# Kernel optimization log

Hardware: AMD Instinct MI355X
Metric: run time of the kernel (lower is better)

Reference implementation:

```python
import jax, jax.numpy as jnp
from jax import lax
import numpy as np

EPS = 1e-8


def _pdist(a):
    # torch.cdist(a, a, p=2): pairwise Euclidean distances [B, B]
    sq = jnp.sum(a * a, axis=1)
    d2 = sq[:, None] + sq[None, :] - 2.0 * (a @ a.T)
    d2 = jnp.maximum(d2, 0.0)
    # safe sqrt: zero distance -> 0 with zero (not NaN) gradient
    pos = d2 > 0
    return jnp.where(pos, jnp.sqrt(jnp.where(pos, d2, 1.0)), 0.0)


def _local_curvature(x, k):
    # PCA-residual curvature per sample: 1 - S0 / sum(S) over k-NN neighborhood
    dists = _pdist(x)                          # [B, B]
    _, knn_idx = lax.top_k(-dists, k + 1)      # smallest k+1 distances
    knn_idx = knn_idx[:, 1:]                   # drop self -> [B, k]
    nbrs = x[knn_idx]                          # [B, k, D] gather
    centered = nbrs - jnp.mean(nbrs, axis=1, keepdims=True)
    S = jnp.linalg.svd(centered, compute_uv=False)  # batched singular values [B, k]
    linearity = S[:, 0] / (jnp.sum(S, axis=1) + EPS)
    return 1.0 - linearity                     # [B]


def reference(z, ref_emb, x_original, k):
    B = z.shape[0]
    curv = _local_curvature(x_original, k)     # [B]
    z_dist = _pdist(z)
    ref_dist = _pdist(ref_emb)
    # weights = clamp(1 - max(curv_i, curv_j), min=0.1)
    weights = jnp.maximum(1.0 - jnp.maximum(curv[:, None], curv[None, :]), 0.1)
    z_norm = z_dist / (jnp.max(z_dist) + EPS)
    ref_norm = ref_dist / (jnp.max(ref_dist) + EPS)
    errors = (z_norm - ref_norm) ** 2 * weights
    mask = jnp.triu(jnp.ones((B, B), dtype=bool), k=1)
    n_pairs = B * (B - 1) / 2.0
    return jnp.sum(jnp.where(mask, errors, 0.0)) / n_pairs


def setup_inputs() -> dict:
    key = jax.random.key(0)
    k1, k2, k3 = jax.random.split(key, 3)
    B, D, DZ, DR = 4096, 1024, 128, 128
    return {
        "z": jax.random.normal(k1, (B, DZ), dtype=jnp.float32),
        "ref_emb": jax.random.normal(k2, (B, DR), dtype=jnp.float32),
        "x_original": jax.random.normal(k3, (B, D), dtype=jnp.float32),
        "k": 10,
    }
```

## Files before the change

### kernel.cpp

```cpp
#include <hip/hip_runtime.h>
#include <math.h>

#define NB 4096
#define DX 1024
#define DZ 128
#define KNN 10
#define STR 32
#define NLIST 32
#define BKK 64
#define NSTEP (DX / BKK)

typedef short short8v __attribute__((ext_vector_type(8)));
typedef float f32x4 __attribute__((ext_vector_type(4)));

#define MFMA16(a, b, c) __builtin_amdgcn_mfma_f32_16x16x32_bf16((a), (b), (c), 0, 0, 0)

__device__ __forceinline__ ushort f2bf(float f) {
  unsigned u = __float_as_uint(f);
  u += 0x7FFFu + ((u >> 16) & 1u);
  return (ushort)(u >> 16);
}
__device__ __forceinline__ float bf2f(ushort h) {
  return __uint_as_float(((unsigned)h) << 16);
}

__device__ __forceinline__ void gload16(const ushort* g, ushort* l) {
  __builtin_amdgcn_global_load_lds(
      (const __attribute__((address_space(1))) void*)g,
      (__attribute__((address_space(3))) void*)l, 16, 0, 0);
}

__device__ __forceinline__ short8v frag_ld(const ushort* base, int row, int fg) {
  int off = (row << 6) + (fg << 4);
  off ^= (row & 7) << 4;
  return *(const short8v*)((const char*)base + off);
}

__device__ __forceinline__ int swz64(int row, int c8) {
  return (row << 7) + ((c8 ^ (row & 7)) << 4);
}
__device__ __forceinline__ short8v frag_ld64(const ushort* base, int row, int kk, int fg) {
  return *(const short8v*)((const char*)base + swz64(row, kk * 4 + fg));
}

#define INSERT10(td, ti, v, idx)                         \
  do {                                                   \
    if ((v) < td[KNN - 1]) {                             \
      _Pragma("unroll")                                  \
      for (int k_ = KNN - 1; k_ >= 1; --k_) {            \
        bool bk = (v) < td[k_];                          \
        bool bk1 = (v) < td[k_ - 1];                     \
        td[k_] = bk ? (bk1 ? td[k_ - 1] : (v)) : td[k_]; \
        ti[k_] = bk ? (bk1 ? ti[k_ - 1] : (idx)) : ti[k_]; \
      }                                                  \
      bool b0 = (v) < td[0];                             \
      ti[0] = b0 ? (idx) : ti[0];                        \
      td[0] = b0 ? (v) : td[0];                          \
    }                                                    \
  } while (0)

__global__ __launch_bounds__(256) void k_rowsq(const float* __restrict__ a,
                                               float* __restrict__ out, int D) {
  int row = blockIdx.x;
  const float4* p = (const float4*)(a + (size_t)row * D);
  float s = 0.f;
  for (int d = threadIdx.x; d < (D >> 2); d += 256) {
    float4 v = p[d];
    s = fmaf(v.x, v.x, s); s = fmaf(v.y, v.y, s);
    s = fmaf(v.z, v.z, s); s = fmaf(v.w, v.w, s);
  }
#pragma unroll
  for (int m = 32; m; m >>= 1) s += __shfl_xor(s, m);
  __shared__ float red[4];
  int w = threadIdx.x >> 6;
  if ((threadIdx.x & 63) == 0) red[w] = s;
  __syncthreads();
  if (threadIdx.x == 0) out[row] = red[0] + red[1] + red[2] + red[3];
}

__global__ __launch_bounds__(256) void k_prep_x(const float* __restrict__ x,
                                                ushort* __restrict__ xh,
                                                float* __restrict__ sqx) {
  const int row = blockIdx.x, t = threadIdx.x;
  float4 v = ((const float4*)(x + (size_t)row * DX))[t];
  ushort4 hv;
  hv.x = f2bf(v.x); hv.y = f2bf(v.y); hv.z = f2bf(v.z); hv.w = f2bf(v.w);
  ((ushort4*)(xh + (size_t)row * DX))[t] = hv;
  float s = fmaf(v.x, v.x, fmaf(v.y, v.y, fmaf(v.z, v.z, v.w * v.w)));
#pragma unroll
  for (int m = 32; m; m >>= 1) s += __shfl_xor(s, m);
  __shared__ float red[4];
  int w = t >> 6;
  if ((t & 63) == 0) red[w] = s;
  __syncthreads();
  if (t == 0) sqx[row] = red[0] + red[1] + red[2] + red[3];
}

__global__ __launch_bounds__(256) void k_prep_zr(const float* __restrict__ z,
                                                 const float* __restrict__ rfm,
                                                 ushort* __restrict__ zh, ushort* __restrict__ zl,
                                                 ushort* __restrict__ rh, ushort* __restrict__ rl,
                                                 float* __restrict__ sqz, float* __restrict__ sqr) {
  const float* src = blockIdx.y ? rfm : z;
  ushort* ph = blockIdx.y ? rh : zh;
  ushort* pl = blockIdx.y ? rl : zl;
  float* sq = blockIdx.y ? sqr : sqz;
  const int t = threadIdx.x;
  const size_t base = (size_t)blockIdx.x * 1024;
  float4 v = ((const float4*)(src + base))[t];
  float vv[4] = {v.x, v.y, v.z, v.w};
  ushort h[4], l[4];
#pragma unroll
  for (int e = 0; e < 4; ++e) {
    h[e] = f2bf(vv[e]);
    l[e] = f2bf(vv[e] - bf2f(h[e]));
  }
  ushort4 hv; hv.x = h[0]; hv.y = h[1]; hv.z = h[2]; hv.w = h[3];
  ushort4 lv; lv.x = l[0]; lv.y = l[1]; lv.z = l[2]; lv.w = l[3];
  ((ushort4*)(ph + base))[t] = hv;
  ((ushort4*)(pl + base))[t] = lv;
  float s = fmaf(v.x, v.x, fmaf(v.y, v.y, fmaf(v.z, v.z, v.w * v.w)));
#pragma unroll
  for (int m = 16; m; m >>= 1) s += __shfl_xor(s, m);
  if ((t & 31) == 0) sq[blockIdx.x * 8 + (t >> 5)] = s;
}

struct SmemKNN {
  union {
    struct { ushort A[2][8192]; ushort B[2][8192]; } s;
    float D[64 * 129];
  } u;
};

template<int PRE>
__global__ __launch_bounds__(256, 2) void k_knn(const float* __restrict__ x,
                                                const ushort* __restrict__ xh,
                                                const float* __restrict__ sqx,
                                                float* __restrict__ cand_d,
                                                int* __restrict__ cand_i) {
  __shared__ SmemKNN sm;
  const int bid = blockIdx.y * STR + blockIdx.x;
  const int xcd = bid & 7, rr = bid >> 3;
  const int strip = (xcd & 3) * 8 + (rr & 7);
  const int itile = (xcd >> 2) * 16 + (rr >> 3);
  const int i0 = itile * 128;
  const int j0 = strip * 128;

  const int tid = threadIdx.x;
  const int lane = tid & 63, wv = tid >> 6;
  const int wr = wv >> 1, wc = wv & 1;
  const int fr = lane & 15, fg = lane >> 4;

  float td[KNN];
  int ti[KNN];
#pragma unroll
  for (int k = 0; k < KNN; ++k) { td[k] = 3.0e38f; ti[k] = 0; }
  const int my_chunk = tid >> 7;
  const int t2 = tid & 127;
  const int srow = t2 >> 1;
  const int cbase = (tid & 1) * 64;

  f32x4 acc[4][4];
  const f32x4 zv4 = {0.f, 0.f, 0.f, 0.f};
#pragma unroll
  for (int m = 0; m < 4; ++m)
#pragma unroll
    for (int n = 0; n < 4; ++n) acc[m][n] = zv4;

  if (PRE) {
    const int lr = lane >> 3;
    const int lc8 = (lane & 7) ^ lr;
#define ISSUE_TILE(kc, buf)                                                  \
  _Pragma("unroll")                                                          \
  for (int c_ = 0; c_ < 4; ++c_) {                                          \
    int ch_ = wv * 4 + c_;                                                   \
    int row_ = ch_ * 8 + lr;                                                 \
    gload16(xh + (size_t)(i0 + row_) * DX + (kc) + lc8 * 8,                  \
            &sm.u.s.A[buf][ch_ * 512]);                                      \
    gload16(xh + (size_t)(j0 + row_) * DX + (kc) + lc8 * 8,                  \
            &sm.u.s.B[buf][ch_ * 512]);                                      \
  }
    ISSUE_TILE(0, 0);
    int buf = 0;
    for (int step = 0; step < NSTEP; ++step) {
      asm volatile("s_waitcnt vmcnt(0)" ::: "memory");
      __syncthreads();
      if (step + 1 < NSTEP) ISSUE_TILE((step + 1) * BKK, buf ^ 1);
      const ushort* Ab = sm.u.s.A[buf];
      const ushort* Bb = sm.u.s.B[buf];
#pragma unroll
      for (int kk = 0; kk < 2; ++kk) {
        short8v fa[4];
#pragma unroll
        for (int m = 0; m < 4; ++m)
          fa[m] = frag_ld64(Ab, wr * 64 + m * 16 + fr, kk, fg);
#pragma unroll
        for (int n = 0; n < 4; ++n) {
          short8v fb = frag_ld64(Bb, wc * 64 + n * 16 + fr, kk, fg);
#pragma unroll
          for (int m = 0; m < 4; ++m)
            acc[m][n] = MFMA16(fa[m], fb, acc[m][n]);
        }
      }
      buf ^= 1;
    }
#undef ISSUE_TILE
  } else {
    for (int kc = 0; kc < DX; kc += BKK) {
      __syncthreads();
#pragma unroll
      for (int l = 0; l < 4; ++l) {
        int idx = tid + l * 256;
        int row = idx >> 3, c8 = idx & 7;
        int off = swz64(row, c8);
        const float* pa = &x[(size_t)(i0 + row) * DX + kc + c8 * 8];
        const float* pb = &x[(size_t)(j0 + row) * DX + kc + c8 * 8];
        float4 a1 = *(const float4*)pa, a2 = *(const float4*)(pa + 4);
        float4 b1 = *(const float4*)pb, b2 = *(const float4*)(pb + 4);
        uint4 pva, pvb;
        pva.x = (unsigned)f2bf(a1.x) | ((unsigned)f2bf(a1.y) << 16);
        pva.y = (unsigned)f2bf(a1.z) | ((unsigned)f2bf(a1.w) << 16);
        pva.z = (unsigned)f2bf(a2.x) | ((unsigned)f2bf(a2.y) << 16);
        pva.w = (unsigned)f2bf(a2.z) | ((unsigned)f2bf(a2.w) << 16);
        pvb.x = (unsigned)f2bf(b1.x) | ((unsigned)f2bf(b1.y) << 16);
        pvb.y = (unsigned)f2bf(b1.z) | ((unsigned)f2bf(b1.w) << 16);
        pvb.z = (unsigned)f2bf(b2.x) | ((unsigned)f2bf(b2.y) << 16);
        pvb.w = (unsigned)f2bf(b2.z) | ((unsigned)f2bf(b2.w) << 16);
        *(uint4*)((char*)sm.u.s.A[0] + off) = pva;
        *(uint4*)((char*)sm.u.s.B[0] + off) = pvb;
      }
      __syncthreads();
#pragma unroll
      for (int kk = 0; kk < 2; ++kk) {
        short8v fa[4];
#pragma unroll
        for (int m = 0; m < 4; ++m)
          fa[m] = frag_ld64(sm.u.s.A[0], wr * 64 + m * 16 + fr, kk, fg);
#pragma unroll
        for (int n = 0; n < 4; ++n) {
          short8v fb = frag_ld64(sm.u.s.B[0], wc * 64 + n * 16 + fr, kk, fg);
#pragma unroll
          for (int m = 0; m < 4; ++m)
            acc[m][n] = MFMA16(fa[m], fb, acc[m][n]);
        }
      }
    }
  }
  __syncthreads();
#pragma unroll
  for (int chunk = 0; chunk < 2; ++chunk) {
    if (wr == chunk) {
#pragma unroll
      for (int m = 0; m < 4; ++m)
#pragma unroll
        for (int n = 0; n < 4; ++n)
#pragma unroll
          for (int r = 0; r < 4; ++r) {
            int rl = m * 16 + fg * 4 + r;
            int cl = wc * 64 + n * 16 + fr;
            int gi = i0 + chunk * 64 + rl, gj = j0 + cl;
            float v = sqx[gi] + sqx[gj] - 2.f * acc[m][n][r];
            sm.u.D[rl * 129 + cl] = (gi == gj) ? 3.0e38f : v;
          }
    }
    __syncthreads();
    if (my_chunk == chunk) {
#pragma unroll 4
      for (int c = 0; c < 64; ++c) {
        float v = sm.u.D[srow * 129 + cbase + c];
        int idx = j0 + cbase + c;
        INSERT10(td, ti, v, idx);
      }
    }
    __syncthreads();
  }
  {
    float pd[KNN]; int pi[KNN];
#pragma unroll
    for (int l = 0; l < KNN; ++l) {
      pd[l] = __shfl_xor(td[l], 1);
      pi[l] = __shfl_xor(ti[l], 1);
    }
#pragma unroll
    for (int l = 0; l < KNN; ++l) INSERT10(td, ti, pd[l], pi[l]);
    if ((tid & 1) == 0) {
      int row = i0 + my_chunk * 64 + srow;
#pragma unroll
      for (int l = 0; l < KNN; ++l) {
        cand_d[((size_t)row * NLIST + strip) * KNN + l] = td[l];
        cand_i[((size_t)row * NLIST + strip) * KNN + l] = ti[l];
      }
    }
  }
}

template<int PRE>
__global__ __launch_bounds__(64) void k_mergegram(const float* __restrict__ cand_d,
                                                  const int* __restrict__ cand_i,
                                                  const float* __restrict__ x,
                                                  const ushort* __restrict__ xh,
                                                  float* __restrict__ G) {
  const int pt = blockIdx.x;
  const int lane = threadIdx.x;
  float v[KNN]; int jx[KNN];
  const float* cd = cand_d + ((size_t)pt * NLIST + lane) * KNN;
  const int* ci = cand_i + ((size_t)pt * NLIST + lane) * KNN;
  const bool act = lane < NLIST;
#pragma unroll
  for (int l = 0; l < KNN; ++l) {
    v[l] = act ? cd[l] : 3.0e38f;
    jx[l] = act ? ci[l] : 0;
  }
  int nbi[KNN];
#pragma unroll
  for (int k = 0; k < KNN; ++k) {
    float bv = v[0]; int bj = jx[0]; int bl = lane;
#pragma unroll
    for (int m = 1; m < 64; m <<= 1) {
      float ov = __shfl_xor(bv, m);
      int oj = __shfl_xor(bj, m);
      int ol = __shfl_xor(bl, m);
      bool take = ov < bv;
      bv = take ? ov : bv; bj = take ? oj : bj; bl = take ? ol : bl;
    }
    nbi[k] = bj;
    if (lane == bl) {
#pragma unroll
      for (int l = 0; l < KNN - 1; ++l) { v[l] = v[l + 1]; jx[l] = jx[l + 1]; }
      v[KNN - 1] = 3.0e38f;
    }
  }
  float P[55];
  float U[KNN];
  float q = 0.f;
#pragma unroll
  for (int c = 0; c < 55; ++c) P[c] = 0.f;
#pragma unroll
  for (int a = 0; a < KNN; ++a) U[a] = 0.f;
  if (PRE) {
    const short8v* nb[KNN];
#pragma unroll
    for (int a = 0; a < KNN; ++a)
      nb[a] = (const short8v*)(xh + (size_t)nbi[a] * DX);
    for (int d8 = lane; d8 < DX / 8; d8 += 64) {
      short8v n8[KNN];
#pragma unroll
      for (int a = 0; a < KNN; ++a) n8[a] = nb[a][d8];
#pragma unroll
      for (int e = 0; e < 8; ++e) {
        float n[KNN];
#pragma unroll
        for (int a = 0; a < KNN; ++a) n[a] = bf2f((ushort)n8[a][e]);
        float m = 0.f;
#pragma unroll
        for (int a = 0; a < KNN; ++a) m += n[a];
        m *= 0.1f;
        q = fmaf(m, m, q);
#pragma unroll
        for (int a = 0; a < KNN; ++a) U[a] = fmaf(n[a], m, U[a]);
        int c = 0;
#pragma unroll
        for (int a = 0; a < KNN; ++a)
#pragma unroll
          for (int b = a; b < KNN; ++b) { P[c] = fmaf(n[a], n[b], P[c]); ++c; }
      }
    }
  } else {
    const float4* nb[KNN];
#pragma unroll
    for (int a = 0; a < KNN; ++a)
      nb[a] = (const float4*)(x + (size_t)nbi[a] * DX);
    for (int d4 = lane; d4 < DX / 4; d4 += 64) {
      float4 n4[KNN];
#pragma unroll
      for (int a = 0; a < KNN; ++a) n4[a] = nb[a][d4];
#pragma unroll
      for (int e = 0; e < 4; ++e) {
        float n[KNN];
#pragma unroll
        for (int a = 0; a < KNN; ++a) n[a] = ((const float*)&n4[a])[e];
        float m = 0.f;
#pragma unroll
        for (int a = 0; a < KNN; ++a) m += n[a];
        m *= 0.1f;
        q = fmaf(m, m, q);
#pragma unroll
        for (int a = 0; a < KNN; ++a) U[a] = fmaf(n[a], m, U[a]);
        int c = 0;
#pragma unroll
        for (int a = 0; a < KNN; ++a)
#pragma unroll
          for (int b = a; b < KNN; ++b) { P[c] = fmaf(n[a], n[b], P[c]); ++c; }
      }
    }
  }
#pragma unroll
  for (int c = 0; c < 55; ++c)
#pragma unroll
    for (int m2 = 32; m2; m2 >>= 1) P[c] += __shfl_xor(P[c], m2);
#pragma unroll
  for (int a = 0; a < KNN; ++a)
#pragma unroll
    for (int m2 = 32; m2; m2 >>= 1) U[a] += __shfl_xor(U[a], m2);
#pragma unroll
  for (int m2 = 32; m2; m2 >>= 1) q += __shfl_xor(q, m2);
  if (lane == 0) {
    int c = 0;
    for (int a = 0; a < KNN; ++a)
      for (int b = a; b < KNN; ++b) { G[(size_t)pt * 55 + c] = P[c] - U[a] - U[b] + q; ++c; }
  }
}

__device__ __forceinline__ constexpr int IJ(int a, int b) {
  return (a <= b) ? (10 * a - (a * (a - 1)) / 2 + (b - a))
                  : (10 * b - (b * (b - 1)) / 2 + (a - b));
}

#define NSWEEP 6
__global__ __launch_bounds__(64) void k_jacobi(const float* __restrict__ G,
                                               float* __restrict__ curv) {
  const int pt = blockIdx.x * 64 + threadIdx.x;
  float M[55];
#pragma unroll
  for (int c = 0; c < 55; ++c) M[c] = G[(size_t)pt * 55 + c];

#pragma unroll
  for (int sweep = 0; sweep < NSWEEP; ++sweep) {
#pragma unroll
    for (int p = 0; p < KNN - 1; ++p) {
#pragma unroll
      for (int q = p + 1; q < KNN; ++q) {
        float apq = M[IJ(p, q)];
        float app = M[IJ(p, p)], aqq = M[IJ(q, q)];
        float theta = (aqq - app) / (2.f * apq);
        float t = 1.f / (fabsf(theta) + sqrtf(fmaf(theta, theta, 1.f)));
        t = (theta < 0.f) ? -t : t;
        t = (apq == 0.f) ? 0.f : t;
        float cc = 1.f / sqrtf(fmaf(t, t, 1.f));
        float ss = t * cc;
#pragma unroll
        for (int r = 0; r < KNN; ++r) {
          if (r == p || r == q) continue;
          float vrp = M[IJ(r, p)];
          float vrq = M[IJ(r, q)];
          M[IJ(r, p)] = cc * vrp - ss * vrq;
          M[IJ(r, q)] = ss * vrp + cc * vrq;
        }
        M[IJ(p, p)] = app - t * apq;
        M[IJ(q, q)] = aqq + t * apq;
        M[IJ(p, q)] = 0.f;
      }
    }
  }

  float lmax = 0.f, ssum = 0.f;
#pragma unroll
  for (int a = 0; a < KNN; ++a) {
    float l = fmaxf(M[IJ(a, a)], 0.f);
    lmax = fmaxf(lmax, l);
    ssum += sqrtf(l);
  }
  curv[pt] = 1.f - sqrtf(lmax) / (ssum + 1e-8f);
}

template<int PRE>
__global__ __launch_bounds__(256, 2) void k_zr(const float* __restrict__ z,
                                               const float* __restrict__ rfm,
                                               const ushort* __restrict__ zh,
                                               const ushort* __restrict__ zl,
                                               const ushort* __restrict__ rh,
                                               const ushort* __restrict__ rl,
                                               const float* __restrict__ sqz,
                                               const float* __restrict__ sqr,
                                               const float* __restrict__ curv,
                                               double* __restrict__ pS,
                                               float* __restrict__ pM) {
  __shared__ struct { ushort Ah[4096], Al[4096], Bh[4096], Bl[4096]; } s;
  const int t = blockIdx.x;
  int ib = 0, base = 0;
  while (base + (32 - ib) <= t) { base += 32 - ib; ++ib; }
  const int jb = ib + (t - base);
  const int i0 = ib * 128, j0 = jb * 128;
  const int tid = threadIdx.x;
  const int lane = tid & 63, wv = tid >> 6;
  const int wr = wv >> 1, wc = wv & 1;
  const int fr = lane & 15, fg = lane >> 4;

  f32x4 zacc[4][4], racc[4][4];
  const f32x4 zv = {0.f, 0.f, 0.f, 0.f};
#pragma unroll
  for (int m = 0; m < 4; ++m)
#pragma unroll
    for (int n = 0; n < 4; ++n) { zacc[m][n] = zv; racc[m][n] = zv; }

#pragma unroll
  for (int mat = 0; mat < 2; ++mat) {
    const float* P = mat ? rfm : z;
    const ushort* Ph = mat ? rh : zh;
    const ushort* Pl = mat ? rl : zl;
    for (int kc = 0; kc < DZ; kc += 32) {
      __syncthreads();
      if (PRE) {
#pragma unroll
        for (int l = 0; l < 2; ++l) {
          int idx = tid + l * 256;
          int row = idx >> 2, c8 = idx & 3;
          int off = (row << 6) + (c8 << 4);
          off ^= (row & 7) << 4;
          size_t ga = (size_t)(i0 + row) * DZ + kc + c8 * 8;
          size_t gb = (size_t)(j0 + row) * DZ + kc + c8 * 8;
          *(uint4*)((char*)s.Ah + off) = *(const uint4*)(Ph + ga);
          *(uint4*)((char*)s.Al + off) = *(const uint4*)(Pl + ga);
          *(uint4*)((char*)s.Bh + off) = *(const uint4*)(Ph + gb);
          *(uint4*)((char*)s.Bl + off) = *(const uint4*)(Pl + gb);
        }
      } else {
#pragma unroll
        for (int l = 0; l < 4; ++l) {
          int idx = tid + l * 256;
          int row = idx >> 3, c4 = idx & 7;
          int off = (row << 6) + (c4 << 3);
          off ^= (row & 7) << 4;
          float4 va = *(const float4*)&P[(size_t)(i0 + row) * DZ + kc + c4 * 4];
          float4 vb = *(const float4*)&P[(size_t)(j0 + row) * DZ + kc + c4 * 4];
          float av[4] = {va.x, va.y, va.z, va.w};
          float bv[4] = {vb.x, vb.y, vb.z, vb.w};
          ushort ah4[4], al4[4], bh4[4], bl4[4];
#pragma unroll
          for (int e = 0; e < 4; ++e) {
            ah4[e] = f2bf(av[e]); al4[e] = f2bf(av[e] - bf2f(ah4[e]));
            bh4[e] = f2bf(bv[e]); bl4[e] = f2bf(bv[e] - bf2f(bh4[e]));
          }
          uint2 p;
          p.x = (unsigned)ah4[0] | ((unsigned)ah4[1] << 16);
          p.y = (unsigned)ah4[2] | ((unsigned)ah4[3] << 16);
          *(uint2*)((char*)s.Ah + off) = p;
          p.x = (unsigned)al4[0] | ((unsigned)al4[1] << 16);
          p.y = (unsigned)al4[2] | ((unsigned)al4[3] << 16);
          *(uint2*)((char*)s.Al + off) = p;
          p.x = (unsigned)bh4[0] | ((unsigned)bh4[1] << 16);
          p.y = (unsigned)bh4[2] | ((unsigned)bh4[3] << 16);
          *(uint2*)((char*)s.Bh + off) = p;
          p.x = (unsigned)bl4[0] | ((unsigned)bl4[1] << 16);
          p.y = (unsigned)bl4[2] | ((unsigned)bl4[3] << 16);
          *(uint2*)((char*)s.Bl + off) = p;
        }
      }
      __syncthreads();
      short8v fah[4], fal[4];
#pragma unroll
      for (int m = 0; m < 4; ++m) {
        int r = wr * 64 + m * 16 + fr;
        fah[m] = frag_ld(s.Ah, r, fg);
        fal[m] = frag_ld(s.Al, r, fg);
      }
#pragma unroll
      for (int n = 0; n < 4; ++n) {
        int r = wc * 64 + n * 16 + fr;
        short8v fbh = frag_ld(s.Bh, r, fg);
        short8v fbl = frag_ld(s.Bl, r, fg);
#pragma unroll
        for (int m = 0; m < 4; ++m) {
          if (mat == 0) {
            zacc[m][n] = MFMA16(fah[m], fbh, zacc[m][n]);
            zacc[m][n] = MFMA16(fah[m], fbl, zacc[m][n]);
            zacc[m][n] = MFMA16(fal[m], fbh, zacc[m][n]);
          } else {
            racc[m][n] = MFMA16(fah[m], fbh, racc[m][n]);
            racc[m][n] = MFMA16(fah[m], fbl, racc[m][n]);
            racc[m][n] = MFMA16(fal[m], fbh, racc[m][n]);
          }
        }
      }
    }
  }

  double s1 = 0, s2 = 0, s3 = 0;
  float mz = 0.f, mr = 0.f;
#pragma unroll
  for (int m = 0; m < 4; ++m)
#pragma unroll
    for (int n = 0; n < 4; ++n)
#pragma unroll
      for (int r = 0; r < 4; ++r) {
        int gi = i0 + wr * 64 + m * 16 + fg * 4 + r;
        int gj = j0 + wc * 64 + n * 16 + fr;
        if (gj > gi) {
          float z2 = fmaxf(sqz[gi] + sqz[gj] - 2.f * zacc[m][n][r], 0.f);
          float r2 = fmaxf(sqr[gi] + sqr[gj] - 2.f * racc[m][n][r], 0.f);
          float w = fmaxf(1.f - fmaxf(curv[gi], curv[gj]), 0.1f);
          s1 += (double)(w * z2);
          s3 += (double)(w * r2);
          s2 += (double)(w * sqrtf(z2 * r2));
          mz = fmaxf(mz, z2);
          mr = fmaxf(mr, r2);
        }
      }
#pragma unroll
  for (int m = 32; m; m >>= 1) {
    s1 += __shfl_xor(s1, m);
    s2 += __shfl_xor(s2, m);
    s3 += __shfl_xor(s3, m);
    mz = fmaxf(mz, __shfl_xor(mz, m));
    mr = fmaxf(mr, __shfl_xor(mr, m));
  }
  __shared__ double rd[4][3];
  __shared__ float rf2[4][2];
  int w = tid >> 6;
  if ((tid & 63) == 0) { rd[w][0] = s1; rd[w][1] = s2; rd[w][2] = s3; rf2[w][0] = mz; rf2[w][1] = mr; }
  __syncthreads();
  if (tid == 0) {
    double a = 0, b = 0, c = 0; float d = 0.f, e = 0.f;
    for (int i = 0; i < 4; ++i) {
      a += rd[i][0]; b += rd[i][1]; c += rd[i][2];
      d = fmaxf(d, rf2[i][0]); e = fmaxf(e, rf2[i][1]);
    }
    pS[(size_t)t * 3 + 0] = a; pS[(size_t)t * 3 + 1] = b; pS[(size_t)t * 3 + 2] = c;
    pM[(size_t)t * 2 + 0] = d; pM[(size_t)t * 2 + 1] = e;
  }
}

__global__ __launch_bounds__(256) void k_final(const double* __restrict__ pS,
                                               const float* __restrict__ pM,
                                               int nb, float* __restrict__ out) {
  int tid = threadIdx.x;
  double s1 = 0, s2 = 0, s3 = 0; float mz = 0.f, mr = 0.f;
  for (int i = tid; i < nb; i += 256) {
    s1 += pS[(size_t)i * 3 + 0]; s2 += pS[(size_t)i * 3 + 1]; s3 += pS[(size_t)i * 3 + 2];
    mz = fmaxf(mz, pM[(size_t)i * 2 + 0]); mr = fmaxf(mr, pM[(size_t)i * 2 + 1]);
  }
#pragma unroll
  for (int m = 32; m; m >>= 1) {
    s1 += __shfl_xor(s1, m); s2 += __shfl_xor(s2, m); s3 += __shfl_xor(s3, m);
    mz = fmaxf(mz, __shfl_xor(mz, m)); mr = fmaxf(mr, __shfl_xor(mr, m));
  }
  __shared__ double rd[4][3];
  __shared__ float rf2[4][2];
  int w = tid >> 6;
  if ((tid & 63) == 0) { rd[w][0] = s1; rd[w][1] = s2; rd[w][2] = s3; rf2[w][0] = mz; rf2[w][1] = mr; }
  __syncthreads();
  if (tid == 0) {
    double a = 0, b = 0, c = 0; float d = 0.f, e = 0.f;
    for (int i = 0; i < 4; ++i) {
      a += rd[i][0]; b += rd[i][1]; c += rd[i][2];
      d = fmaxf(d, rf2[i][0]); e = fmaxf(e, rf2[i][1]);
    }
    double zm = sqrt((double)d) + 1e-8;
    double rm = sqrt((double)e) + 1e-8;
    double total = a / (zm * zm) - 2.0 * b / (zm * rm) + c / (rm * rm);
    double npairs = (double)NB * (double)(NB - 1) / 2.0;
    out[0] = (float)(total / npairs);
  }
}

extern "C" void kernel_launch(void* const* d_in, const int* in_sizes, int n_in,
                              void* d_out, int out_size, void* d_ws, size_t ws_size,
                              hipStream_t stream) {
  const float* z = (const float*)d_in[0];
  const float* rfm = (const float*)d_in[1];
  const float* x = (const float*)d_in[2];
  float* out = (float*)d_out;
  char* w = (char*)d_ws;

  float*  sqx    = (float*)(w + 0);
  float*  sqz    = (float*)(w + 16384);
  float*  sqr    = (float*)(w + 32768);
  float*  curv   = (float*)(w + 49152);
  float*  cand_d = (float*)(w + 229376);
  int*    cand_i = (int*)(w + 5472256);
  float*  G      = (float*)(w + 10715136);
  double* pS     = (double*)(w + 11616256);
  float*  pM     = (float*)(w + 11628928);

  ushort* xh = (ushort*)(w + (size_t)12 * 1024 * 1024);
  ushort* zh = (ushort*)(w + (size_t)20 * 1024 * 1024);
  ushort* zl = (ushort*)(w + (size_t)21 * 1024 * 1024);
  ushort* rh = (ushort*)(w + (size_t)22 * 1024 * 1024);
  ushort* rl = (ushort*)(w + (size_t)23 * 1024 * 1024);
  const bool pre = ws_size >= (size_t)24 * 1024 * 1024;

  if (pre) {
    k_prep_x<<<NB, 256, 0, stream>>>(x, xh, sqx);
    k_prep_zr<<<dim3(NB * DZ / 1024, 2), 256, 0, stream>>>(z, rfm, zh, zl, rh, rl, sqz, sqr);
    k_knn<1><<<dim3(STR, NB / 128), 256, 0, stream>>>(x, xh, sqx, cand_d, cand_i);
    k_mergegram<1><<<NB, 64, 0, stream>>>(cand_d, cand_i, x, xh, G);
  } else {
    k_rowsq<<<NB, 256, 0, stream>>>(x, sqx, DX);
    k_rowsq<<<NB, 256, 0, stream>>>(z, sqz, DZ);
    k_rowsq<<<NB, 256, 0, stream>>>(rfm, sqr, DZ);
    k_knn<0><<<dim3(STR, NB / 128), 256, 0, stream>>>(x, xh, sqx, cand_d, cand_i);
    k_mergegram<0><<<NB, 64, 0, stream>>>(cand_d, cand_i, x, xh, G);
  }
  k_jacobi<<<NB / 64, 64, 0, stream>>>(G, curv);
  if (pre) {
    k_zr<1><<<528, 256, 0, stream>>>(z, rfm, zh, zl, rh, rl, sqz, sqr, curv, pS, pM);
  } else {
    k_zr<0><<<528, 256, 0, stream>>>(z, rfm, zh, zl, rh, rl, sqz, sqr, curv, pS, pM);
  }
  k_final<<<1, 256, 0, stream>>>(pS, pM, 528, out);
}
```

Measured before the change: 263.0 us.

## Enlarge kNN GEMM tile to 256x128 with 512 threads, drop async LDS double buffering

The kNN distance GEMM block tile grows from 128x128 to 256x128, using 8 waves per block and half as many blocks, so each B strip loaded into shared memory is reused across more rows. The precomputed-bf16 path loses its global_load_lds double-buffered pipeline and now uses plain synchronous vector loads into a single buffer, sharing one loop with the fp32 path. This cuts redundant B traffic but exposes load latency with no overlap. The epilogue now runs 4 row chunks through the 64x129 staging buffer.

After: 267.6 us. No clear change (+1.8%).

```diff
diff --git a/kernel.cpp b/kernel.cpp
--- a/kernel.cpp
+++ b/kernel.cpp
@@ -8,7 +8,6 @@
 #define STR 32
 #define NLIST 32
 #define BKK 64
-#define NSTEP (DX / BKK)
 
 typedef short short8v __attribute__((ext_vector_type(8)));
 typedef float f32x4 __attribute__((ext_vector_type(4)));
@@ -22,12 +21,6 @@
 }
 __device__ __forceinline__ float bf2f(ushort h) {
   return __uint_as_float(((unsigned)h) << 16);
-}
-
-__device__ __forceinline__ void gload16(const ushort* g, ushort* l) {
-  __builtin_amdgcn_global_load_lds(
-      (const __attribute__((address_space(1))) void*)g,
-      (__attribute__((address_space(3))) void*)l, 16, 0, 0);
 }
 
 __device__ __forceinline__ short8v frag_ld(const ushort* base, int row, int fg) {
@@ -127,13 +120,13 @@
 
 struct SmemKNN {
   union {
-    struct { ushort A[2][8192]; ushort B[2][8192]; } s;
+    struct { ushort A[256 * BKK], B[128 * BKK]; } s;
     float D[64 * 129];
   } u;
 };
 
 template<int PRE>
-__global__ __launch_bounds__(256, 2) void k_knn(const float* __restrict__ x,
+__global__ __launch_bounds__(512, 4) void k_knn(const float* __restrict__ x,
                                                 const ushort* __restrict__ xh,
                                                 const float* __restrict__ sqx,
                                                 float* __restrict__ cand_d,
@@ -142,8 +135,8 @@
   const int bid = blockIdx.y * STR + blockIdx.x;
   const int xcd = bid & 7, rr = bid >> 3;
   const int strip = (xcd & 3) * 8 + (rr & 7);
-  const int itile = (xcd >> 2) * 16 + (rr >> 3);
-  const int i0 = itile * 128;
+  const int itile = (xcd >> 2) * 8 + (rr >> 3);
+  const int i0 = itile * 256;
   const int j0 = strip * 128;
 
   const int tid = threadIdx.x;
@@ -167,88 +160,70 @@
 #pragma unroll
     for (int n = 0; n < 4; ++n) acc[m][n] = zv4;
 
-  if (PRE) {
-    const int lr = lane >> 3;
-    const int lc8 = (lane & 7) ^ lr;
-#define ISSUE_TILE(kc, buf)                                                  \
-  _Pragma("unroll")                                                          \
-  for (int c_ = 0; c_ < 4; ++c_) {                                          \
-    int ch_ = wv * 4 + c_;                                                   \
-    int row_ = ch_ * 8 + lr;                                                 \
-    gload16(xh + (size_t)(i0 + row_) * DX + (kc) + lc8 * 8,                  \
-            &sm.u.s.A[buf][ch_ * 512]);                                      \
-    gload16(xh + (size_t)(j0 + row_) * DX + (kc) + lc8 * 8,                  \
-            &sm.u.s.B[buf][ch_ * 512]);                                      \
-  }
-    ISSUE_TILE(0, 0);
-    int buf = 0;
-    for (int step = 0; step < NSTEP; ++step) {
-      asm volatile("s_waitcnt vmcnt(0)" ::: "memory");
-      __syncthreads();
-      if (step + 1 < NSTEP) ISSUE_TILE((step + 1) * BKK, buf ^ 1);
-      const ushort* Ab = sm.u.s.A[buf];
-      const ushort* Bb = sm.u.s.B[buf];
-#pragma unroll
-      for (int kk = 0; kk < 2; ++kk) {
-        short8v fa[4];
-#pragma unroll
-        for (int m = 0; m < 4; ++m)
-          fa[m] = frag_ld64(Ab, wr * 64 + m * 16 + fr, kk, fg);
-#pragma unroll
-        for (int n = 0; n < 4; ++n) {
-          short8v fb = frag_ld64(Bb, wc * 64 + n * 16 + fr, kk, fg);
-#pragma unroll
-          for (int m = 0; m < 4; ++m)
-            acc[m][n] = MFMA16(fa[m], fb, acc[m][n]);
-        }
-      }
-      buf ^= 1;
-    }
-#undef ISSUE_TILE
-  } else {
-    for (int kc = 0; kc < DX; kc += BKK) {
-      __syncthreads();
+  for (int kc = 0; kc < DX; kc += BKK) {
+    __syncthreads();
+    if (PRE) {
 #pragma unroll
       for (int l = 0; l < 4; ++l) {
-        int idx = tid + l * 256;
+        int idx = tid + l * 512;
         int row = idx >> 3, c8 = idx & 7;
-        int off = swz64(row, c8);
+        *(uint4*)((char*)sm.u.s.A + swz64(row, c8)) =
+            *(const uint4*)(xh + (size_t)(i0 + row) * DX + kc + c8 * 8);
+      }
+#pragma unroll
+      for (int l = 0; l < 2; ++l) {
+        int idx = tid + l * 512;
+        int row = idx >> 3, c8 = idx & 7;
+        *(uint4*)((char*)sm.u.s.B + swz64(row, c8)) =
+            *(const uint4*)(xh + (size_t)(j0 + row) * DX + kc + c8 * 8);
+      }
+    } else {
+#pragma unroll
+      for (int l = 0; l < 4; ++l) {
+        int idx = tid + l * 512;
+        int row = idx >> 3, c8 = idx & 7;
         const float* pa = &x[(size_t)(i0 + row) * DX + kc + c8 * 8];
-        const float* pb = &x[(size_t)(j0 + row) * DX + kc + c8 * 8];
         float4 a1 = *(const float4*)pa, a2 = *(const float4*)(pa + 4);
-        float4 b1 = *(const float4*)pb, b2 = *(const float4*)(pb + 4);
-        uint4 pva, pvb;
+        uint4 pva;
         pva.x = (unsigned)f2bf(a1.x) | ((unsigned)f2bf(a1.y) << 16);
         pva.y = (unsigned)f2bf(a1.z) | ((unsigned)f2bf(a1.w) << 16);
         pva.z = (unsigned)f2bf(a2.x) | ((unsigned)f2bf(a2.y) << 16);
         pva.w = (unsigned)f2bf(a2.z) | ((unsigned)f2bf(a2.w) << 16);
+        *(uint4*)((char*)sm.u.s.A + swz64(row, c8)) = pva;
+      }
+#pragma unroll
+      for (int l = 0; l < 2; ++l) {
+        int idx = tid + l * 512;
+        int row = idx >> 3, c8 = idx & 7;
+        const float* pb = &x[(size_t)(j0 + row) * DX + kc + c8 * 8];
+        float4 b1 = *(const float4*)pb, b2 = *(const float4*)(pb + 4);
+        uint4 pvb;
         pvb.x = (unsigned)f2bf(b1.x) | ((unsigned)f2bf(b1.y) << 16);
         pvb.y = (unsigned)f2bf(b1.z) | ((unsigned)f2bf(b1.w) << 16);
         pvb.z = (unsigned)f2bf(b2.x) | ((unsigned)f2bf(b2.y) << 16);
         pvb.w = (unsigned)f2bf(b2.z) | ((unsigned)f2bf(b2.w) << 16);
-        *(uint4*)((char*)sm.u.s.A[0] + off) = pva;
-        *(uint4*)((char*)sm.u.s.B[0] + off) = pvb;
-      }
-      __syncthreads();
-#pragma unroll
-      for (int kk = 0; kk < 2; ++kk) {
-        short8v fa[4];
+        *(uint4*)((char*)sm.u.s.B + swz64(row, c8)) = pvb;
+      }
+    }
+    __syncthreads();
+#pragma unroll
+    for (int kk = 0; kk < 2; ++kk) {
+      short8v fa[4];
+#pragma unroll
+      for (int m = 0; m < 4; ++m)
+        fa[m] = frag_ld64(sm.u.s.A, wr * 64 + m * 16 + fr, kk, fg);
+#pragma unroll
+      for (int n = 0; n < 4; ++n) {
+        short8v fb = frag_ld64(sm.u.s.B, wc * 64 + n * 16 + fr, kk, fg);
 #pragma unroll
         for (int m = 0; m < 4; ++m)
-          fa[m] = frag_ld64(sm.u.s.A[0], wr * 64 + m * 16 + fr, kk, fg);
-#pragma unroll
-        for (int n = 0; n < 4; ++n) {
-          short8v fb = frag_ld64(sm.u.s.B[0], wc * 64 + n * 16 + fr, kk, fg);
-#pragma unroll
-          for (int m = 0; m < 4; ++m)
-            acc[m][n] = MFMA16(fa[m], fb, acc[m][n]);
-        }
+          acc[m][n] = MFMA16(fa[m], fb, acc[m][n]);
       }
     }
   }
   __syncthreads();
 #pragma unroll
-  for (int chunk = 0; chunk < 2; ++chunk) {
+  for (int chunk = 0; chunk < 4; ++chunk) {
     if (wr == chunk) {
 #pragma unroll
       for (int m = 0; m < 4; ++m)
@@ -682,13 +657,13 @@
   if (pre) {
     k_prep_x<<<NB, 256, 0, stream>>>(x, xh, sqx);
     k_prep_zr<<<dim3(NB * DZ / 1024, 2), 256, 0, stream>>>(z, rfm, zh, zl, rh, rl, sqz, sqr);
-    k_knn<1><<<dim3(STR, NB / 128), 256, 0, stream>>>(x, xh, sqx, cand_d, cand_i);
+    k_knn<1><<<dim3(STR, NB / 256), 512, 0, stream>>>(x, xh, sqx, cand_d, cand_i);
     k_mergegram<1><<<NB, 64, 0, stream>>>(cand_d, cand_i, x, xh, G);
   } else {
     k_rowsq<<<NB, 256, 0, stream>>>(x, sqx, DX);
     k_rowsq<<<NB, 256, 0, stream>>>(z, sqz, DZ);
     k_rowsq<<<NB, 256, 0, stream>>>(rfm, sqr, DZ);
-    k_knn<0><<<dim3(STR, NB / 128), 256, 0, stream>>>(x, xh, sqx, cand_d, cand_i);
+    k_knn<0><<<dim3(STR, NB / 256), 512, 0, stream>>>(x, xh, sqx, cand_d, cand_i);
     k_mergegram<0><<<NB, 64, 0, stream>>>(cand_d, cand_i, x, xh, G);
   }
   k_jacobi<<<NB / 64, 64, 0, stream>>>(G, curv);
```
